# Optimization experiments

Hardware: AMD Instinct MI355X
Metric: run time of the kernel (lower is better)

The kernel has to match this reference:

```python
import jax, jax.numpy as jnp
import numpy as np

N, E, H = 20000, 320000, 2
F_IN, D, D_OUT, NMID = 17, 64, 32, 18
SLOPE, EPS = 0.2, 1e-5


def _gat(x, Wl, bl, Wr, br, att, bias, src, dst, n, h, c):
    # PyG GATv2Conv, heads=h, concat=False (mean over heads)
    xl = (x @ Wl + bl).reshape(n, h, c)   # source transform
    xr = (x @ Wr + br).reshape(n, h, c)   # target transform
    e = jax.nn.leaky_relu(xl[src] + xr[dst], SLOPE)        # [E,h,c]
    logit = jnp.sum(e * att, axis=-1)                       # [E,h]
    m = jax.ops.segment_max(logit, dst, num_segments=n)    # per-dst softmax
    a = jnp.exp(logit - m[dst])
    s = jax.ops.segment_sum(a, dst, num_segments=n)
    alpha = a / s[dst]
    out = jax.ops.segment_sum(alpha[..., None] * xl[src], dst, num_segments=n)
    return out.mean(axis=1) + bias


def _bn(x, g, b):
    # BatchNorm1d in training mode (batch statistics, biased variance)
    mu = x.mean(axis=0)
    var = jnp.mean((x - mu) ** 2, axis=0)
    return g * (x - mu) * jax.lax.rsqrt(var + EPS) + b


def setup_inputs() -> dict:
    key = jax.random.key(0)
    ks = iter(jax.random.split(key, 64))
    r = lambda *s: jax.random.normal(next(ks), s, jnp.float32) * 0.1
    return dict(
        x=jax.random.normal(next(ks), (N, F_IN), jnp.float32),
        src=jax.random.randint(next(ks), (E,), 0, N),
        dst=jax.random.randint(next(ks), (E,), 0, N),
        W0l=r(F_IN, H * D), b0l=r(H * D), W0r=r(F_IN, H * D), b0r=r(H * D),
        att0=r(H, D), bias0=r(D), g0=jnp.ones((D,), jnp.float32), be0=jnp.zeros((D,), jnp.float32),
        Wml=r(NMID, D, H * D), bml=r(NMID, H * D), Wmr=r(NMID, D, H * D), bmr=r(NMID, H * D),
        attm=r(NMID, H, D), biasm=r(NMID, D), gm=jnp.ones((NMID, D), jnp.float32), bem=jnp.zeros((NMID, D), jnp.float32),
        WLl=r(D, H * D_OUT), bLl=r(H * D_OUT), WLr=r(D, H * D_OUT), bLr=r(H * D_OUT),
        attL=r(H, D_OUT), biasL=r(D_OUT), gL=jnp.ones((D_OUT,), jnp.float32), beL=jnp.zeros((D_OUT,), jnp.float32),
        Wimp=r(D_OUT, 1), bimp=r(1), Wpol=r(D_OUT, 1), bpol=r(1),
    )


def reference(x, src, dst, W0l, b0l, W0r, b0r, att0, bias0, g0, be0,
              Wml, bml, Wmr, bmr, attm, biasm, gm, bem,
              WLl, bLl, WLr, bLr, attL, biasL, gL, beL,
              Wimp, bimp, Wpol, bpol):
    n = x.shape[0]
    loop = jnp.arange(n, dtype=src.dtype)  # add_self_loops=True (PyG default)
    s = jnp.concatenate([src, loop])
    d = jnp.concatenate([dst, loop])
    h = jax.nn.relu(_bn(_gat(x, W0l, b0l, W0r, b0r, att0, bias0, s, d, n, H, D), g0, be0))
    for i in range(NMID):
        h = h + jax.nn.relu(_bn(_gat(h, Wml[i], bml[i], Wmr[i], bmr[i], attm[i], biasm[i], s, d, n, H, D), gm[i], bem[i]))
    h = jax.nn.relu(_bn(_gat(h, WLl, bLl, WLr, bLr, attL, biasL, s, d, n, H, D_OUT), gL, beL))
    return (h @ Wimp + bimp, jax.nn.sigmoid(h @ Wpol + bpol))
```

## Files before the change

### kernel.cpp

```cpp
#include <hip/hip_runtime.h>
#include <math.h>

#define NN 20000
#define NE 320000
#define ET (NE + NN)
#define FIN 17
#define DD 64
#define DOUTC 32
#define NMIDL 18
#define SLOPE 0.2f
#define BN_EPS 1e-5f


__global__ void k_init(int* __restrict__ deg, float* __restrict__ s0, float* __restrict__ s1) {
    int i = blockIdx.x * blockDim.x + threadIdx.x;
    if (i < NN) deg[i] = 1;
    if (i < 128) { s0[i] = 0.f; s1[i] = 0.f; }
}

__global__ void k_hist(const int* __restrict__ dst, int* __restrict__ deg) {
    int i = blockIdx.x * blockDim.x + threadIdx.x;
    if (i < NE) atomicAdd(&deg[dst[i]], 1);
}

__global__ __launch_bounds__(1024) void k_scan(const int* __restrict__ deg,
                                               int* __restrict__ row_ptr,
                                               int* __restrict__ cursor) {
    __shared__ int sarr[1024];
    int t = threadIdx.x;
    const int CH = 20;
    int base = t * CH;
    int sum = 0;
    for (int j = 0; j < CH; ++j) {
        int idx = base + j;
        if (idx < NN) sum += deg[idx];
    }
    sarr[t] = sum;
    __syncthreads();
    for (int off = 1; off < 1024; off <<= 1) {
        int v = (t >= off) ? sarr[t - off] : 0;
        __syncthreads();
        sarr[t] += v;
        __syncthreads();
    }
    int run = sarr[t] - sum;
    for (int j = 0; j < CH; ++j) {
        int idx = base + j;
        if (idx < NN) {
            row_ptr[idx] = run;
            cursor[idx] = run;
            run += deg[idx];
        }
    }
    if (t == 0) row_ptr[NN] = ET;
}

__global__ void k_scatter(const int* __restrict__ src, const int* __restrict__ dst,
                          int* __restrict__ cursor, int* __restrict__ edge_src) {
    int i = blockIdx.x * blockDim.x + threadIdx.x;
    if (i < NE) {
        int d = dst[i];
        int pos = atomicAdd(&cursor[d], 1);
        edge_src[pos] = src[i];
    } else if (i < ET) {
        int v = i - NE;
        int pos = atomicAdd(&cursor[v], 1);
        edge_src[pos] = v;
    }
}


template<int DIN, int DCOLS>
__global__ __launch_bounds__(256) void k_gemm2(const float* __restrict__ hin,
                                               const float* __restrict__ Wl, const float* __restrict__ bl,
                                               const float* __restrict__ Wr, const float* __restrict__ br,
                                               float* __restrict__ xl, float* __restrict__ xr) {
    constexpr int WPN = (2 * DCOLS) / 64;
    constexpr int NPI = 4 / WPN;
    int wave = threadIdx.x >> 6, lane = threadIdx.x & 63;
    int cg = wave % WPN;
    int nsub = wave / WPN;
    int col = cg * 64 + lane;
    bool isl = col < DCOLS;
    const float* W = isl ? Wl : Wr;
    float* xo = isl ? xl : xr;
    int cw = col & (DCOLS - 1);
    float wreg[DIN];
    #pragma unroll
    for (int k = 0; k < DIN; ++k) wreg[k] = W[k * DCOLS + cw];
    float bias = (isl ? bl : br)[cw];

    for (int node0 = blockIdx.x * NPI; node0 < NN; node0 += gridDim.x * NPI) {
        int node = node0 + nsub;
        int nu = __builtin_amdgcn_readfirstlane(node);
        const float* hrow = hin + (size_t)nu * DIN;
        float a0 = 0.f, a1 = 0.f, a2 = 0.f, a3 = 0.f;
        #pragma unroll
        for (int k = 0; k < DIN; k += 4) {
            a0 = fmaf(hrow[k], wreg[k], a0);
            if (k + 1 < DIN) a1 = fmaf(hrow[k + 1], wreg[k + 1], a1);
            if (k + 2 < DIN) a2 = fmaf(hrow[k + 2], wreg[k + 2], a2);
            if (k + 3 < DIN) a3 = fmaf(hrow[k + 3], wreg[k + 3], a3);
        }
        xo[(size_t)node * DCOLS + cw] = ((a0 + a1) + (a2 + a3)) + bias;
    }
}


template<int CPL>
__global__ __launch_bounds__(256) void k_edge2(const float* __restrict__ xl,
                                               const float* __restrict__ xr,
                                               const float* __restrict__ att,
                                               const float* __restrict__ bias,
                                               const int* __restrict__ row_ptr,
                                               const int* __restrict__ edge_src,
                                               float* __restrict__ g) {
    constexpr int HC = CPL * 32;
    constexpr int RS = 2 * HC;
    int wave = threadIdx.x >> 6, lane = threadIdx.x & 63;
    int node = blockIdx.x * 4 + wave;
    if (node >= NN) return;
    int co = lane * CPL;
    float2 xrv, attc;
    if (CPL == 2) {
        xrv  = *(const float2*)&xr[node * RS + co];
        attc = *(const float2*)&att[co];
    } else {
        xrv.x = xr[node * RS + co]; xrv.y = 0.f;
        attc.x = att[co];           attc.y = 0.f;
    }
    int beg = row_ptr[node], end = row_ptr[node + 1];
    float m = -1e30f, s = 0.f;
    float2 o = {0.f, 0.f};

    for (int cb = beg; cb < end; cb += 64) {
        int idx = cb + lane;
        int eload = edge_src[idx < end ? idx : end - 1];
        int cnt = min(64, end - cb);
        for (int b = 0; b < cnt; b += 4) {
            int nb = min(4, cnt - b);
            float p[4]; float2 xv[4];
            #pragma unroll
            for (int j = 0; j < 4; ++j) {
                int u = __shfl(eload, b + (j < nb ? j : 0));
                float2 v;
                if (CPL == 2) v = *(const float2*)&xl[u * RS + co];
                else { v.x = xl[u * RS + co]; v.y = 0.f; }
                xv[j] = v;
                float tx = v.x + xrv.x, ty = v.y + xrv.y;
                tx = tx > 0.f ? tx : SLOPE * tx;
                ty = ty > 0.f ? ty : SLOPE * ty;
                float pp = tx * attc.x + ty * attc.y;
                #pragma unroll
                for (int msk = 16; msk; msk >>= 1) pp += __shfl_xor(pp, msk);
                p[j] = (j < nb) ? pp : -1e30f;
            }
            float nm = fmaxf(fmaxf(fmaxf(p[0], p[1]), fmaxf(p[2], p[3])), m);
            float sc = __expf(m - nm);
            float w0 = __expf(p[0] - nm), w1 = __expf(p[1] - nm);
            float w2 = __expf(p[2] - nm), w3 = __expf(p[3] - nm);
            s = s * sc + (w0 + w1) + (w2 + w3);
            o.x = o.x * sc + w0 * xv[0].x + w1 * xv[1].x + w2 * xv[2].x + w3 * xv[3].x;
            o.y = o.y * sc + w0 * xv[0].y + w1 * xv[1].y + w2 * xv[2].y + w3 * xv[3].y;
            m = nm;
        }
    }
    float inv = 1.f / s;
    float rx = o.x * inv, ry = o.y * inv;
    float ox = __shfl_xor(rx, 32);
    float oy = __shfl_xor(ry, 32);
    if (lane < 32) {
        if (CPL == 2) {
            float2 bv = *(const float2*)&bias[co];
            float2 outv = { 0.5f * (rx + ox) + bv.x, 0.5f * (ry + oy) + bv.y };
            *(float2*)&g[node * HC + co] = outv;
        } else {
            g[node * HC + co] = 0.5f * (rx + ox) + bias[co];
        }
    }
}


__global__ __launch_bounds__(256) void k_stat(const float* __restrict__ g, float* __restrict__ stats, int hc) {
    __shared__ float ls[4][64], ls2[4][64];
    int lane = threadIdx.x & 63;
    int grp  = threadIdx.x >> 6;
    bool act = lane < hc;
    float s = 0.f, s2 = 0.f;
    for (int row = blockIdx.x * 4 + grp; row < NN; row += gridDim.x * 4) {
        float v = act ? g[row * hc + lane] : 0.f;
        s += v; s2 += v * v;
    }
    ls[grp][lane] = s; ls2[grp][lane] = s2;
    __syncthreads();
    if (grp == 0 && act) {
        float ts  = ls[0][lane] + ls[1][lane] + ls[2][lane] + ls[3][lane];
        float ts2 = ls2[0][lane] + ls2[1][lane] + ls2[2][lane] + ls2[3][lane];
        atomicAdd(&stats[lane], ts);
        atomicAdd(&stats[64 + lane], ts2);
    }
}


__global__ void k_apply(const float* __restrict__ g, const float* __restrict__ stats,
                        const float* __restrict__ gam, const float* __restrict__ bet,
                        const float* __restrict__ hin, float* __restrict__ hout,
                        int hc, int addres, float* __restrict__ statsNext) {
    if (blockIdx.x == 0 && threadIdx.x < 128) statsNext[threadIdx.x] = 0.f;
    int i = blockIdx.x * blockDim.x + threadIdx.x;
    int total = NN * hc;
    if (i >= total) return;
    int c = i & (hc - 1);
    float mu  = stats[c] * (1.f / NN);
    float var = stats[64 + c] * (1.f / NN) - mu * mu;
    float rsd = rsqrtf(var + BN_EPS);
    float v = gam[c] * (g[i] - mu) * rsd + bet[c];
    v = (v > 0.f) ? v : 0.f;
    hout[i] = (addres ? hin[i] : 0.f) + v;
}


__global__ void k_head(const float* __restrict__ h,
                       const float* __restrict__ Wimp, const float* __restrict__ bimp,
                       const float* __restrict__ Wpol, const float* __restrict__ bpol,
                       float* __restrict__ out) {
    int n = blockIdx.x * blockDim.x + threadIdx.x;
    if (n >= NN) return;
    float a1 = bimp[0], a2 = bpol[0];
    for (int k = 0; k < DOUTC; ++k) {
        float hv = h[n * DOUTC + k];
        a1 += hv * Wimp[k];
        a2 += hv * Wpol[k];
    }
    out[n] = a1;
    out[NN + n] = 1.f / (1.f + expf(-a2));
}


extern "C" void kernel_launch(void* const* d_in, const int* in_sizes, int n_in,
                              void* d_out, int out_size, void* d_ws, size_t ws_size,
                              hipStream_t stream) {
    const float* x    = (const float*)d_in[0];
    const int*   src  = (const int*)d_in[1];
    const int*   dst  = (const int*)d_in[2];
    const float* W0l  = (const float*)d_in[3];
    const float* b0l  = (const float*)d_in[4];
    const float* W0r  = (const float*)d_in[5];
    const float* b0r  = (const float*)d_in[6];
    const float* att0 = (const float*)d_in[7];
    const float* bias0= (const float*)d_in[8];
    const float* g0   = (const float*)d_in[9];
    const float* be0  = (const float*)d_in[10];
    const float* Wml  = (const float*)d_in[11];
    const float* bml  = (const float*)d_in[12];
    const float* Wmr  = (const float*)d_in[13];
    const float* bmr  = (const float*)d_in[14];
    const float* attm = (const float*)d_in[15];
    const float* biasm= (const float*)d_in[16];
    const float* gm   = (const float*)d_in[17];
    const float* bem  = (const float*)d_in[18];
    const float* WLl  = (const float*)d_in[19];
    const float* bLl  = (const float*)d_in[20];
    const float* WLr  = (const float*)d_in[21];
    const float* bLr  = (const float*)d_in[22];
    const float* attL = (const float*)d_in[23];
    const float* biasL= (const float*)d_in[24];
    const float* gL   = (const float*)d_in[25];
    const float* beL  = (const float*)d_in[26];
    const float* Wimp = (const float*)d_in[27];
    const float* bimp = (const float*)d_in[28];
    const float* Wpol = (const float*)d_in[29];
    const float* bpol = (const float*)d_in[30];
    float* out = (float*)d_out;

    char* w = (char*)d_ws;
    size_t off = 0;
    auto alloc = [&](size_t bytes) -> char* {
        char* p = w + off;
        off += (bytes + 511) & ~(size_t)511;
        return p;
    };
    int* deg      = (int*)alloc(NN * 4);
    int* cursor   = (int*)alloc(NN * 4);
    int* row_ptr  = (int*)alloc((NN + 1) * 4);
    int* edge_src = (int*)alloc(ET * 4);
    float* xl   = (float*)alloc((size_t)NN * 128 * 4);
    float* xr   = (float*)alloc((size_t)NN * 128 * 4);
    float* gbuf = (float*)alloc((size_t)NN * 64 * 4);
    float* hbuf = (float*)alloc((size_t)NN * 64 * 4);
    float* hL   = (float*)alloc((size_t)NN * 32 * 4);
    float* sb[2];
    sb[0] = (float*)alloc(512);
    sb[1] = (float*)alloc(512);

    k_init<<<(NN + 255) / 256, 256, 0, stream>>>(deg, sb[0], sb[1]);
    k_hist<<<(NE + 255) / 256, 256, 0, stream>>>(dst, deg);
    k_scan<<<1, 1024, 0, stream>>>(deg, row_ptr, cursor);
    k_scatter<<<(ET + 255) / 256, 256, 0, stream>>>(src, dst, cursor, edge_src);

    k_gemm2<FIN, 128><<<1536, 256, 0, stream>>>(x, W0l, b0l, W0r, b0r, xl, xr);
    k_edge2<2><<<(NN + 3) / 4, 256, 0, stream>>>(xl, xr, att0, bias0, row_ptr, edge_src, gbuf);
    k_stat<<<256, 256, 0, stream>>>(gbuf, sb[0], DD);
    k_apply<<<(NN * DD + 255) / 256, 256, 0, stream>>>(gbuf, sb[0], g0, be0, nullptr, hbuf, DD, 0, sb[1]);

    for (int i = 0; i < NMIDL; ++i) {
        int L = i + 1;
        const float* Wl = Wml + (size_t)i * DD * 128;
        const float* blp = bml + (size_t)i * 128;
        const float* Wr = Wmr + (size_t)i * DD * 128;
        const float* brp = bmr + (size_t)i * 128;
        const float* at = attm + (size_t)i * 128;
        const float* bs = biasm + (size_t)i * DD;
        const float* ga = gm + (size_t)i * DD;
        const float* be = bem + (size_t)i * DD;
        k_gemm2<DD, 128><<<1536, 256, 0, stream>>>(hbuf, Wl, blp, Wr, brp, xl, xr);
        k_edge2<2><<<(NN + 3) / 4, 256, 0, stream>>>(xl, xr, at, bs, row_ptr, edge_src, gbuf);
        k_stat<<<256, 256, 0, stream>>>(gbuf, sb[L & 1], DD);
        k_apply<<<(NN * DD + 255) / 256, 256, 0, stream>>>(gbuf, sb[L & 1], ga, be, hbuf, hbuf, DD, 1, sb[(L + 1) & 1]);
    }

    {
        int L = 19;
        k_gemm2<DD, 64><<<768, 256, 0, stream>>>(hbuf, WLl, bLl, WLr, bLr, xl, xr);
        k_edge2<1><<<(NN + 3) / 4, 256, 0, stream>>>(xl, xr, attL, biasL, row_ptr, edge_src, gbuf);
        k_stat<<<256, 256, 0, stream>>>(gbuf, sb[L & 1], DOUTC);
        k_apply<<<(NN * DOUTC + 255) / 256, 256, 0, stream>>>(gbuf, sb[L & 1], gL, beL, nullptr, hL, DOUTC, 0, sb[(L + 1) & 1]);
    }

    k_head<<<(NN + 255) / 256, 256, 0, stream>>>(hL, Wimp, bimp, Wpol, bpol, out);
}
```

Measured before the change: 1.540 ms.

## Register-block GEMM over four nodes and widen edge softmax batches with lazy rescale

```diff
diff --git a/kernel.cpp b/kernel.cpp
--- a/kernel.cpp
+++ b/kernel.cpp
@@ -71,15 +71,17 @@
 
 
 template<int DIN, int DCOLS>
-__global__ __launch_bounds__(256) void k_gemm2(const float* __restrict__ hin,
+__global__ __launch_bounds__(256) void k_gemm3(const float* __restrict__ hin,
                                                const float* __restrict__ Wl, const float* __restrict__ bl,
                                                const float* __restrict__ Wr, const float* __restrict__ br,
                                                float* __restrict__ xl, float* __restrict__ xr) {
-    constexpr int WPN = (2 * DCOLS) / 64;
-    constexpr int NPI = 4 / WPN;
-    int wave = threadIdx.x >> 6, lane = threadIdx.x & 63;
-    int cg = wave % WPN;
-    int nsub = wave / WPN;
+    constexpr int CG = (2 * DCOLS) / 64;
+    constexpr int NSETS = 4 / CG;
+    constexpr int NPB = NSETS * 4;
+    int wave = __builtin_amdgcn_readfirstlane(threadIdx.x >> 6);
+    int lane = threadIdx.x & 63;
+    int cg = wave % CG;
+    int nset = wave / CG;
     int col = cg * 64 + lane;
     bool isl = col < DCOLS;
     const float* W = isl ? Wl : Wr;
@@ -90,36 +92,37 @@
     for (int k = 0; k < DIN; ++k) wreg[k] = W[k * DCOLS + cw];
     float bias = (isl ? bl : br)[cw];
 
-    for (int node0 = blockIdx.x * NPI; node0 < NN; node0 += gridDim.x * NPI) {
-        int node = node0 + nsub;
-        int nu = __builtin_amdgcn_readfirstlane(node);
-        const float* hrow = hin + (size_t)nu * DIN;
+    for (int n0 = blockIdx.x * NPB + nset * 4; n0 < NN; n0 += gridDim.x * NPB) {
+        const float* h0 = hin + (size_t)n0 * DIN;
         float a0 = 0.f, a1 = 0.f, a2 = 0.f, a3 = 0.f;
-        #pragma unroll
-        for (int k = 0; k < DIN; k += 4) {
-            a0 = fmaf(hrow[k], wreg[k], a0);
-            if (k + 1 < DIN) a1 = fmaf(hrow[k + 1], wreg[k + 1], a1);
-            if (k + 2 < DIN) a2 = fmaf(hrow[k + 2], wreg[k + 2], a2);
-            if (k + 3 < DIN) a3 = fmaf(hrow[k + 3], wreg[k + 3], a3);
+        #pragma unroll 16
+        for (int k = 0; k < DIN; ++k) {
+            float wk = wreg[k];
+            a0 = fmaf(h0[k],           wk, a0);
+            a1 = fmaf(h0[DIN + k],     wk, a1);
+            a2 = fmaf(h0[2 * DIN + k], wk, a2);
+            a3 = fmaf(h0[3 * DIN + k], wk, a3);
         }
-        xo[(size_t)node * DCOLS + cw] = ((a0 + a1) + (a2 + a3)) + bias;
+        xo[(size_t)(n0 + 0) * DCOLS + cw] = a0 + bias;
+        xo[(size_t)(n0 + 1) * DCOLS + cw] = a1 + bias;
+        xo[(size_t)(n0 + 2) * DCOLS + cw] = a2 + bias;
+        xo[(size_t)(n0 + 3) * DCOLS + cw] = a3 + bias;
     }
 }
 
 
 template<int CPL>
-__global__ __launch_bounds__(256) void k_edge2(const float* __restrict__ xl,
-                                               const float* __restrict__ xr,
-                                               const float* __restrict__ att,
-                                               const float* __restrict__ bias,
-                                               const int* __restrict__ row_ptr,
-                                               const int* __restrict__ edge_src,
-                                               float* __restrict__ g) {
+__global__ __launch_bounds__(64) void k_edge3(const float* __restrict__ xl,
+                                              const float* __restrict__ xr,
+                                              const float* __restrict__ att,
+                                              const float* __restrict__ bias,
+                                              const int* __restrict__ row_ptr,
+                                              const int* __restrict__ edge_src,
+                                              float* __restrict__ g) {
     constexpr int HC = CPL * 32;
     constexpr int RS = 2 * HC;
-    int wave = threadIdx.x >> 6, lane = threadIdx.x & 63;
-    int node = blockIdx.x * 4 + wave;
-    if (node >= NN) return;
+    int lane = threadIdx.x;
+    int node = blockIdx.x;
     int co = lane * CPL;
     float2 xrv, attc;
     if (CPL == 2) {
@@ -137,11 +140,11 @@
         int idx = cb + lane;
         int eload = edge_src[idx < end ? idx : end - 1];
         int cnt = min(64, end - cb);
-        for (int b = 0; b < cnt; b += 4) {
-            int nb = min(4, cnt - b);
-            float p[4]; float2 xv[4];
+        for (int b = 0; b < cnt; b += 8) {
+            int nb = min(8, cnt - b);
+            float p[8]; float2 xv[8];
             #pragma unroll
-            for (int j = 0; j < 4; ++j) {
+            for (int j = 0; j < 8; ++j) {
                 int u = __shfl(eload, b + (j < nb ? j : 0));
                 float2 v;
                 if (CPL == 2) v = *(const float2*)&xl[u * RS + co];
@@ -155,14 +158,22 @@
                 for (int msk = 16; msk; msk >>= 1) pp += __shfl_xor(pp, msk);
                 p[j] = (j < nb) ? pp : -1e30f;
             }
-            float nm = fmaxf(fmaxf(fmaxf(p[0], p[1]), fmaxf(p[2], p[3])), m);
-            float sc = __expf(m - nm);
-            float w0 = __expf(p[0] - nm), w1 = __expf(p[1] - nm);
-            float w2 = __expf(p[2] - nm), w3 = __expf(p[3] - nm);
-            s = s * sc + (w0 + w1) + (w2 + w3);
-            o.x = o.x * sc + w0 * xv[0].x + w1 * xv[1].x + w2 * xv[2].x + w3 * xv[3].x;
-            o.y = o.y * sc + w0 * xv[0].y + w1 * xv[1].y + w2 * xv[2].y + w3 * xv[3].y;
-            m = nm;
+            float nm = fmaxf(fmaxf(fmaxf(p[0], p[1]), fmaxf(p[2], p[3])),
+                             fmaxf(fmaxf(p[4], p[5]), fmaxf(p[6], p[7])));
+            if (nm > m + 8.f) {
+                float sc = __expf(m - nm);
+                s *= sc; o.x *= sc; o.y *= sc;
+                m = nm;
+            }
+            float w0 = __expf(p[0] - m), w1 = __expf(p[1] - m);
+            float w2 = __expf(p[2] - m), w3 = __expf(p[3] - m);
+            float w4 = __expf(p[4] - m), w5 = __expf(p[5] - m);
+            float w6 = __expf(p[6] - m), w7 = __expf(p[7] - m);
+            s += ((w0 + w1) + (w2 + w3)) + ((w4 + w5) + (w6 + w7));
+            o.x += ((w0 * xv[0].x + w1 * xv[1].x) + (w2 * xv[2].x + w3 * xv[3].x))
+                 + ((w4 * xv[4].x + w5 * xv[5].x) + (w6 * xv[6].x + w7 * xv[7].x));
+            o.y += ((w0 * xv[0].y + w1 * xv[1].y) + (w2 * xv[2].y + w3 * xv[3].y))
+                 + ((w4 * xv[4].y + w5 * xv[5].y) + (w6 * xv[6].y + w7 * xv[7].y));
         }
     }
     float inv = 1.f / s;
@@ -298,8 +309,8 @@
     k_scan<<<1, 1024, 0, stream>>>(deg, row_ptr, cursor);
     k_scatter<<<(ET + 255) / 256, 256, 0, stream>>>(src, dst, cursor, edge_src);
 
-    k_gemm2<FIN, 128><<<1536, 256, 0, stream>>>(x, W0l, b0l, W0r, b0r, xl, xr);
-    k_edge2<2><<<(NN + 3) / 4, 256, 0, stream>>>(xl, xr, att0, bias0, row_ptr, edge_src, gbuf);
+    k_gemm3<FIN, 128><<<1250, 256, 0, stream>>>(x, W0l, b0l, W0r, b0r, xl, xr);
+    k_edge3<2><<<NN, 64, 0, stream>>>(xl, xr, att0, bias0, row_ptr, edge_src, gbuf);
     k_stat<<<256, 256, 0, stream>>>(gbuf, sb[0], DD);
     k_apply<<<(NN * DD + 255) / 256, 256, 0, stream>>>(gbuf, sb[0], g0, be0, nullptr, hbuf, DD, 0, sb[1]);
 
@@ -313,16 +324,16 @@
         const float* bs = biasm + (size_t)i * DD;
         const float* ga = gm + (size_t)i * DD;
         const float* be = bem + (size_t)i * DD;
-        k_gemm2<DD, 128><<<1536, 256, 0, stream>>>(hbuf, Wl, blp, Wr, brp, xl, xr);
-        k_edge2<2><<<(NN + 3) / 4, 256, 0, stream>>>(xl, xr, at, bs, row_ptr, edge_src, gbuf);
+        k_gemm3<DD, 128><<<1250, 256, 0, stream>>>(hbuf, Wl, blp, Wr, brp, xl, xr);
+        k_edge3<2><<<NN, 64, 0, stream>>>(xl, xr, at, bs, row_ptr, edge_src, gbuf);
         k_stat<<<256, 256, 0, stream>>>(gbuf, sb[L & 1], DD);
         k_apply<<<(NN * DD + 255) / 256, 256, 0, stream>>>(gbuf, sb[L & 1], ga, be, hbuf, hbuf, DD, 1, sb[(L + 1) & 1]);
     }
 
     {
         int L = 19;
-        k_gemm2<DD, 64><<<768, 256, 0, stream>>>(hbuf, WLl, bLl, WLr, bLr, xl, xr);
-        k_edge2<1><<<(NN + 3) / 4, 256, 0, stream>>>(xl, xr, attL, biasL, row_ptr, edge_src, gbuf);
+        k_gemm3<DD, 64><<<1250, 256, 0, stream>>>(hbuf, WLl, bLl, WLr, bLr, xl, xr);
+        k_edge3<1><<<NN, 64, 0, stream>>>(xl, xr, attL, biasL, row_ptr, edge_src, gbuf);
         k_stat<<<256, 256, 0, stream>>>(gbuf, sb[L & 1], DOUTC);
         k_apply<<<(NN * DOUTC + 255) / 256, 256, 0, stream>>>(gbuf, sb[L & 1], gL, beL, nullptr, hL, DOUTC, 0, sb[(L + 1) & 1]);
     }
```

Result: slower. 2.236 ms (+45.2%).
